# Performance work log

Hardware: AMD Instinct MI355X
Metric: run time of the kernel (lower is better)

## Reference

```python
import jax, jax.numpy as jnp
import numpy as np

M_DIM = 256  # attention key dim, used for 1/sqrt(M) scaling


def sparsemax(z):
    # z: [..., F]. Martins & Astudillo sparsemax along last axis.
    F = z.shape[-1]
    zs = -jnp.sort(-z, axis=-1)                      # sorted descending
    css = jnp.cumsum(zs, axis=-1)                    # cumulative sums
    r = jnp.arange(1, F + 1, dtype=z.dtype)
    support = zs * r > (css - 1.0)                   # k(z) condition
    k = jnp.sum(support, axis=-1, keepdims=True)     # support size >= 1
    css_k = jnp.take_along_axis(css, k.astype(jnp.int32) - 1, axis=-1)
    tau = (css_k - 1.0) / k.astype(z.dtype)          # threshold
    return jnp.maximum(z - tau, 0.0)


def setup_inputs() -> dict:
    key = jax.random.key(0)
    ks = jax.random.split(key, 5)
    B, D, F, M = 4096, 1024, 8192, M_DIM
    bound = 0.01
    x = jax.random.normal(ks[0], (B, D), dtype=jnp.float32)
    X_data = jax.random.normal(ks[1], (F, D), dtype=jnp.float32)
    Wq = jax.random.uniform(ks[2], (M, D), dtype=jnp.float32, minval=-bound, maxval=bound)
    Wk = jax.random.uniform(ks[3], (M, D), dtype=jnp.float32, minval=-bound, maxval=bound)
    Wv = jax.random.uniform(ks[4], (D, D), dtype=jnp.float32, minval=-2 * bound, maxval=2 * bound)
    return {
        'x': x, 'X_data': X_data,
        'Wq': Wq, 'bq': jnp.zeros((M,), jnp.float32),
        'Wk': Wk, 'bk': jnp.zeros((M,), jnp.float32),
        'Wv': Wv, 'bv': jnp.zeros((D,), jnp.float32),
    }


def reference(x, X_data, Wq, bq, Wk, bk, Wv, bv):
    M = Wq.shape[0]
    scale = 1.0 / jnp.sqrt(jnp.asarray(M, x.dtype))
    Q = (x @ Wq.T + bq) * scale            # [B, M]
    K = (X_data @ Wk.T + bk) * scale       # [F, M]
    V = X_data @ Wv.T + bv                 # [F, D]
    scores = Q @ K.T                       # [B, F]  (note: 1/M total scaling, as in source)
    attn = sparsemax(scores)               # [B, F], sparse simplex projection
    x_hat = attn @ V                       # [B, D]
    return (x, x_hat, attn)
```

## Files before the change

kernel.cpp:

```cpp
#include <hip/hip_runtime.h>
#include <cstdint>
#include <cstddef>

typedef __attribute__((ext_vector_type(4))) float f32x4;
typedef __attribute__((ext_vector_type(8))) short bf16x8;
typedef __attribute__((ext_vector_type(4))) unsigned short u16x4;
typedef __attribute__((ext_vector_type(8))) unsigned short u16x8;

#define GPTR(p) ((const __attribute__((address_space(1))) void*)(p))
#define LPTR(p) ((__attribute__((address_space(3))) void*)(p))

static constexpr int BB = 4096;
static constexpr int DD = 1024;
static constexpr int FF = 8192;
static constexpr int MM = 256;

__device__ __forceinline__ unsigned short f2bf(float f) {
    union { float f; unsigned u; } x; x.f = f;
    return (unsigned short)((x.u + 0x7FFFu + ((x.u >> 16) & 1u)) >> 16);
}
__device__ __forceinline__ float bf2f(unsigned short h) {
    union { unsigned u; float f; } x; x.u = ((unsigned)h) << 16;
    return x.f;
}
__device__ __forceinline__ int xcd_swz(int bid, int grid) {
    const int cpx = grid >> 3;
    return (bid & 7) * cpx + (bid >> 3);
}

__global__ __launch_bounds__(256) void cvt_bf16(const float* __restrict__ in,
                                                unsigned short* __restrict__ out, int n) {
    int i = (blockIdx.x * 256 + threadIdx.x) * 4;
    if (i >= n) return;
    f32x4 v = *(const f32x4*)(in + i);
    u16x4 o;
    o.x = f2bf(v.x); o.y = f2bf(v.y); o.z = f2bf(v.z); o.w = f2bf(v.w);
    *(u16x4*)(out + i) = o;
}

template<int Mo, int No, int Kd, int KC, int OUT_BF16, int BIAS_MODE, int TN_FAST>
__global__ __launch_bounds__(256) void gemm_t(
    const unsigned short* __restrict__ A,
    const unsigned short* __restrict__ Bm,
    void* __restrict__ Cout,
    const float* __restrict__ bias, float scale)
{
    constexpr int mt = Mo >> 7, nt = No >> 7;
    constexpr int chunk = Kd / KC;

    __shared__ alignas(16) unsigned short As[128 * 32];
    __shared__ alignas(16) unsigned short Bs[128 * 32];

    const int tid  = threadIdx.x;
    const int lane = tid & 63;
    const int wid  = tid >> 6;
    const int L = xcd_swz(blockIdx.x, KC * mt * nt);
    int tm, tn, kc;
    if constexpr (TN_FAST) {
        tn = (L % nt) << 7; const int r = L / nt;
        tm = (r % mt) << 7; kc = r / mt;
    } else {
        tm = (L % mt) << 7; const int r = L / mt;
        tn = (r % nt) << 7; kc = r / nt;
    }
    const int kbase = kc * chunk;
    const int wm = (wid >> 1) * 64;
    const int wn = (wid & 1) * 64;
    const int lr = lane & 15;
    const int lg = lane >> 4;

    f32x4 acc[4][4] = {};

    const int srow = tid >> 2;
    const int scol = (tid & 3) << 3;
    const unsigned short* aptr = A  + (size_t)(tm + srow) * Kd + kbase + scol;
    const unsigned short* bptr = Bm + (size_t)(tn + srow) * Kd + kbase + scol;
    unsigned short* As_base = &As[wid * 512];
    unsigned short* Bs_base = &Bs[wid * 512];

    for (int k0 = 0; k0 < chunk; k0 += 32) {
        __builtin_amdgcn_global_load_lds(GPTR(aptr + k0),                   LPTR(As_base),        16, 0, 0);
        __builtin_amdgcn_global_load_lds(GPTR(aptr + (size_t)64 * Kd + k0), LPTR(As_base + 2048), 16, 0, 0);
        __builtin_amdgcn_global_load_lds(GPTR(bptr + k0),                   LPTR(Bs_base),        16, 0, 0);
        __builtin_amdgcn_global_load_lds(GPTR(bptr + (size_t)64 * Kd + k0), LPTR(Bs_base + 2048), 16, 0, 0);
        __syncthreads();

        bf16x8 af[4], bfr[4];
        #pragma unroll
        for (int mi = 0; mi < 4; ++mi)
            af[mi] = *(const bf16x8*)&As[(wm + mi * 16 + lr) * 32 + lg * 8];
        #pragma unroll
        for (int ni = 0; ni < 4; ++ni)
            bfr[ni] = *(const bf16x8*)&Bs[(wn + ni * 16 + lr) * 32 + lg * 8];

        #pragma unroll
        for (int mi = 0; mi < 4; ++mi)
            #pragma unroll
            for (int ni = 0; ni < 4; ++ni)
                acc[mi][ni] = __builtin_amdgcn_mfma_f32_16x16x32_bf16(af[mi], bfr[ni], acc[mi][ni], 0, 0, 0);
        __syncthreads();
    }

    if constexpr (KC > 1) {
        unsigned short* Pk = (unsigned short*)Cout + (size_t)kc * Mo * No;
        #pragma unroll
        for (int mi = 0; mi < 4; ++mi)
            #pragma unroll
            for (int ni = 0; ni < 4; ++ni)
                #pragma unroll
                for (int r = 0; r < 4; ++r) {
                    const int row = tm + wm + mi * 16 + lg * 4 + r;
                    const int col = tn + wn + ni * 16 + lr;
                    Pk[(size_t)row * No + col] = f2bf(acc[mi][ni][r]);
                }
    } else {
        #pragma unroll
        for (int mi = 0; mi < 4; ++mi)
            #pragma unroll
            for (int ni = 0; ni < 4; ++ni)
                #pragma unroll
                for (int r = 0; r < 4; ++r) {
                    const int row = tm + wm + mi * 16 + lg * 4 + r;
                    const int col = tn + wn + ni * 16 + lr;
                    float v = acc[mi][ni][r];
                    if (BIAS_MODE == 1) v += bias[col];
                    if (BIAS_MODE == 2) v += bias[row];
                    v *= scale;
                    if (OUT_BF16) ((unsigned short*)Cout)[(size_t)row * No + col] = f2bf(v);
                    else          ((float*)Cout)[(size_t)row * No + col] = v;
                }
    }
}

template<int KC>
__global__ __launch_bounds__(512) void gemm_xhat_256(
    const unsigned short* __restrict__ A,
    const unsigned short* __restrict__ Bm,
    unsigned short* __restrict__ P)
{
    constexpr int KCH = FF / KC;
    constexpr int NT  = KCH / 32;
    constexpr int mt  = BB >> 8;
    constexpr int nt  = DD >> 8;

    __shared__ alignas(16) unsigned short SH[4 * 16384];

    const int tid  = threadIdx.x;
    const int lane = tid & 63;
    const int wid  = tid >> 6;
    const int wr   = wid >> 2;
    const int wc   = wid & 3;
    const int lr   = lane & 15;
    const int lg   = lane >> 4;

    const int L  = xcd_swz(blockIdx.x, KC * mt * nt);
    const int tn = (L % nt) << 8;
    const int r0 = L / nt;
    const int tm = (r0 % mt) << 8;
    const int kc = r0 / mt;
    const size_t kbase = (size_t)kc * KCH;

    const unsigned short* ag0 = A  + (size_t)(tm + (tid >> 2)) * FF + kbase + ((tid & 3) << 3);
    const unsigned short* bg0 = Bm + (size_t)(tn + (tid >> 2)) * FF + kbase + ((tid & 3) << 3);

    auto STAGE_A = [&](int tt) {
        const int buf = tt & 3;
        #pragma unroll
        for (int s = 0; s < 2; ++s)
            __builtin_amdgcn_global_load_lds(GPTR(ag0 + (size_t)(s * 128) * FF + tt * 32),
                LPTR(&SH[buf * 16384 + s * 4096 + wid * 512]), 16, 0, 0);
    };
    auto STAGE_B = [&](int tt) {
        const int buf = tt & 3;
        #pragma unroll
        for (int s = 0; s < 2; ++s)
            __builtin_amdgcn_global_load_lds(GPTR(bg0 + (size_t)(s * 128) * FF + tt * 32),
                LPTR(&SH[buf * 16384 + 8192 + s * 4096 + wid * 512]), 16, 0, 0);
    };

    f32x4 acc[8][4] = {};

    STAGE_A(0); STAGE_B(0);
    STAGE_A(1); STAGE_B(1);
    STAGE_A(2); STAGE_B(2);
    asm volatile("s_waitcnt vmcnt(8)" ::: "memory");
    __builtin_amdgcn_s_barrier();

    #pragma unroll 1
    for (int t = 0; t < NT; ++t) {
        if (t) {
            if (t < NT - 2)      asm volatile("s_waitcnt vmcnt(8)" ::: "memory");
            else if (t == NT-2)  asm volatile("s_waitcnt vmcnt(4)" ::: "memory");
            else                 asm volatile("s_waitcnt vmcnt(0)" ::: "memory");
            __builtin_amdgcn_s_barrier();
        }
        const int buf = t & 3;
        const unsigned short* Ab = &SH[buf * 16384];
        const unsigned short* Bb = &SH[buf * 16384 + 8192];

        bf16x8 bfr[4], af[4];
        #pragma unroll
        for (int ni = 0; ni < 4; ++ni)
            bfr[ni] = *(const bf16x8*)&Bb[(wc * 64 + ni * 16 + lr) * 32 + lg * 8];
        #pragma unroll
        for (int mi = 0; mi < 4; ++mi)
            af[mi] = *(const bf16x8*)&Ab[(wr * 128 + mi * 16 + lr) * 32 + lg * 8];
        if (t + 3 < NT) STAGE_A(t + 3);
        __builtin_amdgcn_sched_barrier(0);
        __builtin_amdgcn_s_setprio(1);
        #pragma unroll
        for (int mi = 0; mi < 4; ++mi)
            #pragma unroll
            for (int ni = 0; ni < 4; ++ni)
                acc[mi][ni] = __builtin_amdgcn_mfma_f32_16x16x32_bf16(af[mi], bfr[ni], acc[mi][ni], 0, 0, 0);
        __builtin_amdgcn_s_setprio(0);
        __builtin_amdgcn_s_barrier();

        bf16x8 af2[4];
        #pragma unroll
        for (int mi = 0; mi < 4; ++mi)
            af2[mi] = *(const bf16x8*)&Ab[(wr * 128 + 64 + mi * 16 + lr) * 32 + lg * 8];
        if (t + 3 < NT) STAGE_B(t + 3);
        __builtin_amdgcn_sched_barrier(0);
        __builtin_amdgcn_s_setprio(1);
        #pragma unroll
        for (int mi = 0; mi < 4; ++mi)
            #pragma unroll
            for (int ni = 0; ni < 4; ++ni)
                acc[4 + mi][ni] = __builtin_amdgcn_mfma_f32_16x16x32_bf16(af2[mi], bfr[ni], acc[4 + mi][ni], 0, 0, 0);
        __builtin_amdgcn_s_setprio(0);
    }

    unsigned short* Pk = P + ((size_t)kc * BB + tm) * DD + tn;
    #pragma unroll
    for (int mi = 0; mi < 8; ++mi)
        #pragma unroll
        for (int ni = 0; ni < 4; ++ni)
            #pragma unroll
            for (int r = 0; r < 4; ++r) {
                const int row = wr * 128 + mi * 16 + lg * 4 + r;
                const int col = wc * 64 + ni * 16 + lr;
                Pk[(size_t)row * DD + col] = f2bf(acc[mi][ni][r]);
            }
}

template<int KC, int MODE>
__global__ __launch_bounds__(256) void reduce_sk(
    const unsigned short* __restrict__ P, void* __restrict__ out,
    const float* __restrict__ bias, size_t total, int NoMask, float scale)
{
    const size_t i = ((size_t)blockIdx.x * 256 + threadIdx.x) * 8;
    float v[8] = {0,0,0,0,0,0,0,0};
    #pragma unroll
    for (int kc = 0; kc < KC; ++kc) {
        u16x8 p = *(const u16x8*)(P + kc * total + i);
        #pragma unroll
        for (int c = 0; c < 8; ++c) v[c] += bf2f(p[c]);
    }
    if (MODE == 1) {
        u16x8 o;
        #pragma unroll
        for (int c = 0; c < 8; ++c)
            o[c] = f2bf((v[c] + bias[(i + c) & NoMask]) * scale);
        *(u16x8*)((unsigned short*)out + i) = o;
    } else {
        f32x4 o0, o1;
        #pragma unroll
        for (int c = 0; c < 4; ++c) { o0[c] = v[c]; o1[c] = v[4 + c]; }
        *(f32x4*)((float*)out + i)     = o0;
        *(f32x4*)((float*)out + i + 4) = o1;
    }
}

__global__ __launch_bounds__(256) void sparsemax_k(unsigned short* __restrict__ SA,
                                                   float* __restrict__ attn)
{
    __shared__ float red[16];
    const int t = threadIdx.x;
    const int w = t >> 6, lane = t & 63;
    unsigned short* Zrow = SA + (size_t)blockIdx.x * FF;
    float* Arow = attn + (size_t)blockIdx.x * FF;

    f32x4 z[8];
    #pragma unroll
    for (int j = 0; j < 4; ++j) {
        u16x8 v = *(const u16x8*)&Zrow[j * 2048 + t * 8];
        #pragma unroll
        for (int c = 0; c < 4; ++c) {
            z[2 * j][c]     = bf2f(v[c]);
            z[2 * j + 1][c] = bf2f(v[4 + c]);
        }
    }

    float mx = -1e30f, sm = 0.0f;
    #pragma unroll
    for (int j = 0; j < 8; ++j)
        #pragma unroll
        for (int c = 0; c < 4; ++c) { mx = fmaxf(mx, z[j][c]); sm += z[j][c]; }
    #pragma unroll
    for (int off = 32; off > 0; off >>= 1) {
        mx = fmaxf(mx, __shfl_xor(mx, off));
        sm += __shfl_xor(sm, off);
    }
    if (lane == 0) { red[w] = mx; red[8 + w] = sm; }
    __syncthreads();
    mx = fmaxf(fmaxf(red[0], red[1]), fmaxf(red[2], red[3]));
    sm = red[8] + red[9] + red[10] + red[11];
    __syncthreads();

    float lo = fmaxf(mx - 1.0f, (sm - 1.0f) * (1.0f / (float)FF));
    float hi = mx - 1.0f / (float)FF;

    for (int it = 0; it < 8; ++it) {
        const float mid = 0.5f * (lo + hi);
        float s = 0.0f;
        #pragma unroll
        for (int j = 0; j < 8; ++j)
            #pragma unroll
            for (int c = 0; c < 4; ++c) s += fmaxf(z[j][c] - mid, 0.0f);
        #pragma unroll
        for (int off = 32; off > 0; off >>= 1) s += __shfl_xor(s, off);
        if (lane == 0) red[w] = s;
        __syncthreads();
        s = red[0] + red[1] + red[2] + red[3];
        __syncthreads();
        if (s >= 1.0f) lo = mid; else hi = mid;
    }

    for (int it = 0; it < 2; ++it) {
        float s = 0.0f, cnt = 0.0f;
        #pragma unroll
        for (int j = 0; j < 8; ++j)
            #pragma unroll
            for (int c = 0; c < 4; ++c) {
                const float v = z[j][c];
                if (v > lo) { s += v; cnt += 1.0f; }
            }
        #pragma unroll
        for (int off = 32; off > 0; off >>= 1) { s += __shfl_xor(s, off); cnt += __shfl_xor(cnt, off); }
        if (lane == 0) { red[w] = s; red[8 + w] = cnt; }
        __syncthreads();
        s   = red[0] + red[1] + red[2] + red[3];
        cnt = red[8] + red[9] + red[10] + red[11];
        __syncthreads();
        lo = (s - 1.0f) / cnt;
    }
    const float tau = lo;

    #pragma unroll
    for (int j = 0; j < 4; ++j) {
        f32x4 a0, a1;
        #pragma unroll
        for (int c = 0; c < 4; ++c) {
            a0[c] = fmaxf(z[2 * j][c] - tau, 0.0f);
            a1[c] = fmaxf(z[2 * j + 1][c] - tau, 0.0f);
        }
        *(f32x4*)&Arow[j * 2048 + t * 8]     = a0;
        *(f32x4*)&Arow[j * 2048 + t * 8 + 4] = a1;
        u16x8 o;
        #pragma unroll
        for (int c = 0; c < 4; ++c) { o[c] = f2bf(a0[c]); o[4 + c] = f2bf(a1[c]); }
        *(u16x8*)&Zrow[j * 2048 + t * 8] = o;
    }
}

extern "C" void kernel_launch(void* const* d_in, const int* in_sizes, int n_in,
                              void* d_out, int out_size, void* d_ws, size_t ws_size,
                              hipStream_t stream) {
    const float* x  = (const float*)d_in[0];
    const float* Xd = (const float*)d_in[1];
    const float* Wq = (const float*)d_in[2];
    const float* bq = (const float*)d_in[3];
    const float* Wk = (const float*)d_in[4];
    const float* bk = (const float*)d_in[5];
    const float* Wv = (const float*)d_in[6];
    const float* bv = (const float*)d_in[7];

    float* out       = (float*)d_out;
    float* out_xhat  = out + (size_t)BB * DD;
    float* out_attn  = out + (size_t)2 * BB * DD;

    char* w = (char*)d_ws;
    unsigned short* xb  = (unsigned short*)w; w += (size_t)BB * DD * 2;
    unsigned short* Xb  = (unsigned short*)w; w += (size_t)FF * DD * 2;
    unsigned short* Wqb = (unsigned short*)w; w += (size_t)MM * DD * 2;
    unsigned short* Wkb = (unsigned short*)w; w += (size_t)MM * DD * 2;
    unsigned short* Wvb = (unsigned short*)w; w += (size_t)DD * DD * 2;
    unsigned short* Qb  = (unsigned short*)w; w += (size_t)BB * MM * 2;
    unsigned short* Kb  = (unsigned short*)w; w += (size_t)FF * MM * 2;
    unsigned short* Vtb = (unsigned short*)w; w += (size_t)DD * FF * 2;
    unsigned short* Sb  = (unsigned short*)w; w += (size_t)BB * FF * 2;

    unsigned short* Pb  = (unsigned short*)d_ws;
    unsigned short* PQ  = (unsigned short*)out_attn;
    unsigned short* PK  = PQ + (size_t)8 * BB * MM;

    hipMemcpyAsync(d_out, d_in[0], (size_t)BB * DD * sizeof(float),
                   hipMemcpyDeviceToDevice, stream);

    cvt_bf16<<<BB * DD / 1024, 256, 0, stream>>>(x,  xb,  BB * DD);
    cvt_bf16<<<FF * DD / 1024, 256, 0, stream>>>(Xd, Xb,  FF * DD);
    cvt_bf16<<<MM * DD / 1024, 256, 0, stream>>>(Wq, Wqb, MM * DD);
    cvt_bf16<<<MM * DD / 1024, 256, 0, stream>>>(Wk, Wkb, MM * DD);
    cvt_bf16<<<DD * DD / 1024, 256, 0, stream>>>(Wv, Wvb, DD * DD);

    const float scl = 0.0625f;

    gemm_t<BB, MM, DD, 8, 0, 0, 0><<<8 * (BB/128) * (MM/128), 256, 0, stream>>>(xb, Wqb, PQ, nullptr, 1.0f);
    gemm_t<FF, MM, DD, 4, 0, 0, 0><<<4 * (FF/128) * (MM/128), 256, 0, stream>>>(Xb, Wkb, PK, nullptr, 1.0f);
    reduce_sk<8, 1><<<BB * MM / 2048, 256, 0, stream>>>(PQ, Qb, bq, (size_t)BB * MM, MM - 1, scl);
    reduce_sk<4, 1><<<FF * MM / 2048, 256, 0, stream>>>(PK, Kb, bk, (size_t)FF * MM, MM - 1, scl);

    gemm_t<DD, FF, DD, 1, 1, 2, 0><<<(DD/128) * (FF/128), 256, 0, stream>>>(Wvb, Xb, Vtb, bv, 1.0f);
    gemm_t<BB, FF, MM, 1, 1, 0, 1><<<(BB/128) * (FF/128), 256, 0, stream>>>(Qb, Kb, Sb, nullptr, 1.0f);
    sparsemax_k<<<BB, 256, 0, stream>>>(Sb, out_attn);
    gemm_xhat_256<4><<<4 * (BB/256) * (DD/256), 512, 0, stream>>>(Sb, Vtb, Pb);
    reduce_sk<4, 0><<<BB * DD / 2048, 256, 0, stream>>>(Pb, out_xhat, nullptr, (size_t)BB * DD, 0, 1.0f);
}
```

Baseline: 254.1 us.

## Route V and score GEMMs through pipelined 256-tile kernel; merge weight conversions

Generalizes the 256x256 multi-buffered x_hat GEMM kernel and uses it for the V projection (split-K by 2 with a new bias-reducing pass) and for the Q·K^T score GEMM. Both previously ran on the simpler 128-tile kernel with a single buffer. The three small weight conversions are also merged into one launch. The V GEMM now writes bf16 partials plus an extra reduce pass, which adds memory traffic and a rounding step in exchange for better MFMA pipelining.

```diff
diff --git a/kernel.cpp b/kernel.cpp
--- a/kernel.cpp
+++ b/kernel.cpp
@@ -38,12 +38,27 @@
     *(u16x4*)(out + i) = o;
 }
 
-template<int Mo, int No, int Kd, int KC, int OUT_BF16, int BIAS_MODE, int TN_FAST>
+__global__ __launch_bounds__(256) void cvt_w(
+    const float* __restrict__ Wq, const float* __restrict__ Wk, const float* __restrict__ Wv,
+    unsigned short* __restrict__ Wqb, unsigned short* __restrict__ Wkb, unsigned short* __restrict__ Wvb)
+{
+    int i = (blockIdx.x * 256 + threadIdx.x) * 4;
+    const float* in; unsigned short* out; int off;
+    if (i < MM * DD)            { in = Wq; out = Wqb; off = 0; }
+    else if (i < 2 * MM * DD)   { in = Wk; out = Wkb; off = MM * DD; }
+    else                        { in = Wv; out = Wvb; off = 2 * MM * DD; }
+    const int j = i - off;
+    f32x4 v = *(const f32x4*)(in + j);
+    u16x4 o;
+    o.x = f2bf(v.x); o.y = f2bf(v.y); o.z = f2bf(v.z); o.w = f2bf(v.w);
+    *(u16x4*)(out + j) = o;
+}
+
+template<int Mo, int No, int Kd, int KC>
 __global__ __launch_bounds__(256) void gemm_t(
     const unsigned short* __restrict__ A,
     const unsigned short* __restrict__ Bm,
-    void* __restrict__ Cout,
-    const float* __restrict__ bias, float scale)
+    unsigned short* __restrict__ P)
 {
     constexpr int mt = Mo >> 7, nt = No >> 7;
     constexpr int chunk = Kd / KC;
@@ -55,14 +70,10 @@
     const int lane = tid & 63;
     const int wid  = tid >> 6;
     const int L = xcd_swz(blockIdx.x, KC * mt * nt);
-    int tm, tn, kc;
-    if constexpr (TN_FAST) {
-        tn = (L % nt) << 7; const int r = L / nt;
-        tm = (r % mt) << 7; kc = r / mt;
-    } else {
-        tm = (L % mt) << 7; const int r = L / mt;
-        tn = (r % nt) << 7; kc = r / nt;
-    }
+    const int tm = (L % mt) << 7;
+    const int r  = L / mt;
+    const int tn = (r % nt) << 7;
+    const int kc = r / nt;
     const int kbase = kc * chunk;
     const int wm = (wid >> 1) * 64;
     const int wn = (wid & 1) * 64;
@@ -101,47 +112,29 @@
         __syncthreads();
     }
 
-    if constexpr (KC > 1) {
-        unsigned short* Pk = (unsigned short*)Cout + (size_t)kc * Mo * No;
-        #pragma unroll
-        for (int mi = 0; mi < 4; ++mi)
-            #pragma unroll
-            for (int ni = 0; ni < 4; ++ni)
-                #pragma unroll
-                for (int r = 0; r < 4; ++r) {
-                    const int row = tm + wm + mi * 16 + lg * 4 + r;
-                    const int col = tn + wn + ni * 16 + lr;
-                    Pk[(size_t)row * No + col] = f2bf(acc[mi][ni][r]);
-                }
-    } else {
-        #pragma unroll
-        for (int mi = 0; mi < 4; ++mi)
-            #pragma unroll
-            for (int ni = 0; ni < 4; ++ni)
-                #pragma unroll
-                for (int r = 0; r < 4; ++r) {
-                    const int row = tm + wm + mi * 16 + lg * 4 + r;
-                    const int col = tn + wn + ni * 16 + lr;
-                    float v = acc[mi][ni][r];
-                    if (BIAS_MODE == 1) v += bias[col];
-                    if (BIAS_MODE == 2) v += bias[row];
-                    v *= scale;
-                    if (OUT_BF16) ((unsigned short*)Cout)[(size_t)row * No + col] = f2bf(v);
-                    else          ((float*)Cout)[(size_t)row * No + col] = v;
-                }
-    }
-}
-
-template<int KC>
-__global__ __launch_bounds__(512) void gemm_xhat_256(
+    unsigned short* Pk = P + (size_t)kc * Mo * No;
+    #pragma unroll
+    for (int mi = 0; mi < 4; ++mi)
+        #pragma unroll
+        for (int ni = 0; ni < 4; ++ni)
+            #pragma unroll
+            for (int r2 = 0; r2 < 4; ++r2) {
+                const int row = tm + wm + mi * 16 + lg * 4 + r2;
+                const int col = tn + wn + ni * 16 + lr;
+                Pk[(size_t)row * No + col] = f2bf(acc[mi][ni][r2]);
+            }
+}
+
+template<int Mo, int No, int Kd, int KC, int DIRECT>
+__global__ __launch_bounds__(512) void gemm256(
     const unsigned short* __restrict__ A,
     const unsigned short* __restrict__ Bm,
-    unsigned short* __restrict__ P)
+    unsigned short* __restrict__ Out)
 {
-    constexpr int KCH = FF / KC;
+    constexpr int KCH = Kd / KC;
     constexpr int NT  = KCH / 32;
-    constexpr int mt  = BB >> 8;
-    constexpr int nt  = DD >> 8;
+    constexpr int mt  = Mo >> 8;
+    constexpr int nt  = No >> 8;
 
     __shared__ alignas(16) unsigned short SH[4 * 16384];
 
@@ -160,21 +153,21 @@
     const int kc = r0 / mt;
     const size_t kbase = (size_t)kc * KCH;
 
-    const unsigned short* ag0 = A  + (size_t)(tm + (tid >> 2)) * FF + kbase + ((tid & 3) << 3);
-    const unsigned short* bg0 = Bm + (size_t)(tn + (tid >> 2)) * FF + kbase + ((tid & 3) << 3);
+    const unsigned short* ag0 = A  + (size_t)(tm + (tid >> 2)) * Kd + kbase + ((tid & 3) << 3);
+    const unsigned short* bg0 = Bm + (size_t)(tn + (tid >> 2)) * Kd + kbase + ((tid & 3) << 3);
 
     auto STAGE_A = [&](int tt) {
         const int buf = tt & 3;
         #pragma unroll
         for (int s = 0; s < 2; ++s)
-            __builtin_amdgcn_global_load_lds(GPTR(ag0 + (size_t)(s * 128) * FF + tt * 32),
+            __builtin_amdgcn_global_load_lds(GPTR(ag0 + (size_t)(s * 128) * Kd + tt * 32),
                 LPTR(&SH[buf * 16384 + s * 4096 + wid * 512]), 16, 0, 0);
     };
     auto STAGE_B = [&](int tt) {
         const int buf = tt & 3;
         #pragma unroll
         for (int s = 0; s < 2; ++s)
-            __builtin_amdgcn_global_load_lds(GPTR(bg0 + (size_t)(s * 128) * FF + tt * 32),
+            __builtin_amdgcn_global_load_lds(GPTR(bg0 + (size_t)(s * 128) * Kd + tt * 32),
                 LPTR(&SH[buf * 16384 + 8192 + s * 4096 + wid * 512]), 16, 0, 0);
     };
 
@@ -231,7 +224,8 @@
         __builtin_amdgcn_s_setprio(0);
     }
 
-    unsigned short* Pk = P + ((size_t)kc * BB + tm) * DD + tn;
+    unsigned short* Ok = DIRECT ? (Out + (size_t)tm * No + tn)
+                                : (Out + ((size_t)kc * Mo + tm) * No + tn);
     #pragma unroll
     for (int mi = 0; mi < 8; ++mi)
         #pragma unroll
@@ -240,11 +234,11 @@
             for (int r = 0; r < 4; ++r) {
                 const int row = wr * 128 + mi * 16 + lg * 4 + r;
                 const int col = wc * 64 + ni * 16 + lr;
-                Pk[(size_t)row * DD + col] = f2bf(acc[mi][ni][r]);
+                Ok[(size_t)row * No + col] = f2bf(acc[mi][ni][r]);
             }
 }
 
-template<int KC, int MODE>
+template<int KC, int MODE, int SHIFT = 0>
 __global__ __launch_bounds__(256) void reduce_sk(
     const unsigned short* __restrict__ P, void* __restrict__ out,
     const float* __restrict__ bias, size_t total, int NoMask, float scale)
@@ -262,6 +256,12 @@
         #pragma unroll
         for (int c = 0; c < 8; ++c)
             o[c] = f2bf((v[c] + bias[(i + c) & NoMask]) * scale);
+        *(u16x8*)((unsigned short*)out + i) = o;
+    } else if (MODE == 2) {
+        const float b = bias[i >> SHIFT];
+        u16x8 o;
+        #pragma unroll
+        for (int c = 0; c < 8; ++c) o[c] = f2bf(v[c] + b);
         *(u16x8*)((unsigned short*)out + i) = o;
     } else {
         f32x4 o0, o1;
@@ -391,29 +391,32 @@
     unsigned short* Vtb = (unsigned short*)w; w += (size_t)DD * FF * 2;
     unsigned short* Sb  = (unsigned short*)w; w += (size_t)BB * FF * 2;
 
-    unsigned short* Pb  = (unsigned short*)d_ws;
-    unsigned short* PQ  = (unsigned short*)out_attn;
-    unsigned short* PK  = PQ + (size_t)8 * BB * MM;
+    unsigned short* Pb = (unsigned short*)d_ws;
+    unsigned short* PV = Sb;
+    unsigned short* PQ = (unsigned short*)out_attn;
+    unsigned short* PK = PQ + (size_t)8 * BB * MM;
 
     hipMemcpyAsync(d_out, d_in[0], (size_t)BB * DD * sizeof(float),
                    hipMemcpyDeviceToDevice, stream);
 
     cvt_bf16<<<BB * DD / 1024, 256, 0, stream>>>(x,  xb,  BB * DD);
     cvt_bf16<<<FF * DD / 1024, 256, 0, stream>>>(Xd, Xb,  FF * DD);
-    cvt_bf16<<<MM * DD / 1024, 256, 0, stream>>>(Wq, Wqb, MM * DD);
-    cvt_bf16<<<MM * DD / 1024, 256, 0, stream>>>(Wk, Wkb, MM * DD);
-    cvt_bf16<<<DD * DD / 1024, 256, 0, stream>>>(Wv, Wvb, DD * DD);
+    cvt_w<<<(2 * MM * DD + DD * DD) / 1024, 256, 0, stream>>>(Wq, Wk, Wv, Wqb, Wkb, Wvb);
 
     const float scl = 0.0625f;
 
-    gemm_t<BB, MM, DD, 8, 0, 0, 0><<<8 * (BB/128) * (MM/128), 256, 0, stream>>>(xb, Wqb, PQ, nullptr, 1.0f);
-    gemm_t<FF, MM, DD, 4, 0, 0, 0><<<4 * (FF/128) * (MM/128), 256, 0, stream>>>(Xb, Wkb, PK, nullptr, 1.0f);
+    gemm_t<BB, MM, DD, 8><<<8 * (BB/128) * (MM/128), 256, 0, stream>>>(xb, Wqb, PQ);
+    gemm_t<FF, MM, DD, 4><<<4 * (FF/128) * (MM/128), 256, 0, stream>>>(Xb, Wkb, PK);
     reduce_sk<8, 1><<<BB * MM / 2048, 256, 0, stream>>>(PQ, Qb, bq, (size_t)BB * MM, MM - 1, scl);
     reduce_sk<4, 1><<<FF * MM / 2048, 256, 0, stream>>>(PK, Kb, bk, (size_t)FF * MM, MM - 1, scl);
 
-    gemm_t<DD, FF, DD, 1, 1, 2, 0><<<(DD/128) * (FF/128), 256, 0, stream>>>(Wvb, Xb, Vtb, bv, 1.0f);
-    gemm_t<BB, FF, MM, 1, 1, 0, 1><<<(BB/128) * (FF/128), 256, 0, stream>>>(Qb, Kb, Sb, nullptr, 1.0f);
+    gemm256<DD, FF, DD, 2, 0><<<2 * (DD/256) * (FF/256), 512, 0, stream>>>(Wvb, Xb, PV);
+    reduce_sk<2, 2, 13><<<DD * FF / 2048, 256, 0, stream>>>(PV, Vtb, bv, (size_t)DD * FF, 0, 1.0f);
+
+    gemm256<BB, FF, MM, 1, 1><<<(BB/256) * (FF/256), 512, 0, stream>>>(Qb, Kb, Sb);
+
     sparsemax_k<<<BB, 256, 0, stream>>>(Sb, out_attn);
-    gemm_xhat_256<4><<<4 * (BB/256) * (DD/256), 512, 0, stream>>>(Sb, Vtb, Pb);
+
+    gemm256<BB, DD, FF, 4, 0><<<4 * (BB/256) * (DD/256), 512, 0, stream>>>(Sb, Vtb, Pb);
     reduce_sk<4, 0><<<BB * DD / 2048, 256, 0, stream>>>(Pb, out_xhat, nullptr, (size_t)BB * DD, 0, 1.0f);
 }
```

Result: no change. 257.3 us (+1.3%).
